# Performance work log

Measured on AMD Instinct MI355X. Metric: run time of the kernel, lower is better.

## Reference

```python
import jax, jax.numpy as jnp
import numpy as np

B, X, Z, E = 65536, 362, 100, 3  # batch, x_dim, z_dim, action_space


def _lin_init(k, fan_in, fan_out):
    kw, kb = jax.random.split(k)
    bound = 1.0 / np.sqrt(fan_in)
    W = jax.random.uniform(kw, (fan_in, fan_out), jnp.float32, -bound, bound)
    b = jax.random.uniform(kb, (fan_out,), jnp.float32, -bound, bound)
    return W, b


def setup_inputs() -> dict:
    key = jax.random.key(0)
    ks = jax.random.split(key, 12)
    batch_x = jax.random.normal(ks[0], (B, X), jnp.float32)
    batch_next = jax.random.normal(ks[1], (B, X), jnp.float32)
    batch_a = jax.random.randint(ks[2], (B,), 0, E, jnp.int32)
    # encoder params
    W1, b1 = _lin_init(ks[3], X, 256)
    W2, b2 = _lin_init(ks[4], 256, 200)
    W3, b3 = _lin_init(ks[5], 200, Z)
    # stacked expert params [E, in, out]
    def stack(k, fi, fo):
        kk = jax.random.split(k, E)
        Ws, bs = zip(*[_lin_init(kk[i], fi, fo) for i in range(E)])
        return jnp.stack(Ws), jnp.stack(bs)
    eW1, eb1 = stack(ks[6], Z, 150)
    eW2, eb2 = stack(ks[7], 150, 250)
    eW3, eb3 = stack(ks[8], 250, 300)
    eW4, eb4 = stack(ks[9], 300, X)
    return dict(batch_x=batch_x, batch_next=batch_next, batch_a=batch_a,
                W1=W1, b1=b1, W2=W2, b2=b2, W3=W3, b3=b3,
                eW1=eW1, eb1=eb1, eW2=eW2, eb2=eb2,
                eW3=eW3, eb3=eb3, eW4=eW4, eb4=eb4)


def reference(batch_x, batch_next, batch_a,
              W1, b1, W2, b2, W3, b3,
              eW1, eb1, eW2, eb2, eW3, eb3, eW4, eb4):
    # encoder: Linear->ReLU->Linear->ReLU->Linear->Sigmoid
    h = jax.nn.relu(batch_x @ W1 + b1)
    h = jax.nn.relu(h @ W2 + b2)
    z = jax.nn.sigmoid(h @ W3 + b3)  # [B, Z]
    # routed experts: run all E experts on the full batch (E=3, small),
    # then select per-sample output by action index (same math as per-sample loop)
    h = jax.nn.relu(jnp.einsum('bz,ezh->ebh', z, eW1) + eb1[:, None, :])
    h = jax.nn.relu(jnp.einsum('ebh,ehk->ebk', h, eW2) + eb2[:, None, :])
    h = jax.nn.relu(jnp.einsum('ebk,ekm->ebm', h, eW3) + eb3[:, None, :])
    pred_all = jnp.einsum('ebm,emx->ebx', h, eW4) + eb4[:, None, :]  # [E, B, X]
    pred = pred_all[batch_a, jnp.arange(batch_a.shape[0])]  # [B, X]
    delta = batch_next - batch_x
    loss = jnp.mean((pred[:, 1:] - delta[:, 1:]) ** 2) \
         + jnp.mean((pred[:, 0] - delta[:, 0]) ** 2)
    return loss
```

## Files before the change

### kernel.cpp

```cpp
#include <hip/hip_runtime.h>
#include <math.h>

#define BATCH 65536
#define XD 362
#define ZD 100

#define WS_IDX_OFF 256
#define WS_WT_OFF  786688

#define OFF_W1 0
#define OFF_W2 98304
#define OFF_W3 163840
#define OFF_E1 192512
#define OFF_E2 290816
#define OFF_E3 413696
#define OFF_E4 708608

#define ROWS 48

typedef short short8 __attribute__((ext_vector_type(8)));
typedef float f32x4 __attribute__((ext_vector_type(4)));

__device__ __forceinline__ unsigned short f2bf(float f) {
    union { float f; unsigned u; } v; v.f = f;
    unsigned u = v.u + 0x7fffu + ((v.u >> 16) & 1u);
    return (unsigned short)(u >> 16);
}
__device__ __forceinline__ float bf2f(unsigned u) {
    union { unsigned u; float f; } v; v.u = u << 16; return v.f;
}

__global__ __launch_bounds__(256) void repack_kernel(
    const float* __restrict__ W1, const float* __restrict__ W2,
    const float* __restrict__ W3, const float* __restrict__ eW1,
    const float* __restrict__ eW2, const float* __restrict__ eW3,
    const float* __restrict__ eW4, unsigned short* __restrict__ dst) {
    int m = blockIdx.y;
    const float* src; int K, N, Kp, Np; size_t off;
    if (m == 0)      { src = W1; K = 362; N = 256; Kp = 384; Np = 256; off = OFF_W1; }
    else if (m == 1) { src = W2; K = 256; N = 200; Kp = 256; Np = 256; off = OFF_W2; }
    else if (m == 2) { src = W3; K = 200; N = 100; Kp = 224; Np = 128; off = OFF_W3; }
    else if (m <= 5) { int e = m - 3;  src = eW1 + e * 15000;  K = 100; N = 150; Kp = 128; Np = 256; off = OFF_E1 + (size_t)e * 32768; }
    else if (m <= 8) { int e = m - 6;  src = eW2 + e * 37500;  K = 150; N = 250; Kp = 160; Np = 256; off = OFF_E2 + (size_t)e * 40960; }
    else if (m <= 11){ int e = m - 9;  src = eW3 + e * 75000;  K = 250; N = 300; Kp = 256; Np = 384; off = OFF_E3 + (size_t)e * 98304; }
    else             { int e = m - 12; src = eW4 + e * 108600; K = 300; N = 362; Kp = 320; Np = 384; off = OFF_E4 + (size_t)e * 122880; }
    int nkt = Kp / 32;
    int total = Kp * Np;
    for (int i = blockIdx.x * 256 + threadIdx.x; i < total; i += gridDim.x * 256) {
        int j = i & 7, lane = (i >> 3) & 63, t = i >> 9;
        int kt = t % nkt, ct = t / nkt;
        int k = kt * 32 + (lane >> 4) * 8 + j;
        int n = ct * 16 + (lane & 15);
        float v = (k < K && n < N) ? src[(size_t)k * N + n] : 0.0f;
        dst[off + i] = f2bf(v);
    }
}

__global__ __launch_bounds__(256) void bucket_kernel(const int* __restrict__ a,
                                                     int* __restrict__ counts,
                                                     int* __restrict__ idxlist) {
    int b = blockIdx.x * 256 + threadIdx.x;
    int lane = threadIdx.x & 63;
    int e = a[b];
    unsigned long long below = (lane == 63) ? ~0ull >> 1
                                            : ((1ull << (lane + 1)) - 1ull) >> 1;
    int pos = 0;
#pragma unroll
    for (int ee = 0; ee < 3; ++ee) {
        unsigned long long mask = __ballot(e == ee);
        if (e == ee) {
            int leader = __ffsll((long long)mask) - 1;
            int base = 0;
            if (lane == leader)
                base = atomicAdd(&counts[ee], __popcll(mask));
            base = __shfl(base, leader, 64);
            pos = base + __popcll(mask & below);
        }
    }
    idxlist[e * BATCH + pos] = b;
}

template <int KP, int NP, int LDI, int LDO, int NREAL, int NSTORE>
__device__ __forceinline__ void mfma_layer(
    const unsigned short* __restrict__ Wf, const float* __restrict__ bias,
    const unsigned short* __restrict__ inL, unsigned short* __restrict__ outL,
    int wv, int lane) {
    constexpr int NKT = KP / 32, NCT = NP / 16, CPW = NCT / 8;
    const int quad = lane >> 4, l15 = lane & 15;
    f32x4 acc[3][CPW];
#pragma unroll
    for (int rt = 0; rt < 3; ++rt)
#pragma unroll
        for (int i = 0; i < CPW; ++i) acc[rt][i] = (f32x4){0.f, 0.f, 0.f, 0.f};
    const unsigned short* ap = inL + l15 * LDI + quad * 8;
    __builtin_amdgcn_s_setprio(1);
#pragma unroll
    for (int kt = 0; kt < NKT; ++kt) {
        short8 a0 = *(const short8*)(ap + kt * 32);
        short8 a1 = *(const short8*)(ap + 16 * LDI + kt * 32);
        short8 a2 = *(const short8*)(ap + 32 * LDI + kt * 32);
        short8 bf[CPW];
#pragma unroll
        for (int i = 0; i < CPW; ++i)
            bf[i] = *(const short8*)(Wf + ((size_t)((wv + 8 * i) * NKT + kt) * 64 + lane) * 8);
#pragma unroll
        for (int i = 0; i < CPW; ++i) {
            acc[0][i] = __builtin_amdgcn_mfma_f32_16x16x32_bf16(a0, bf[i], acc[0][i], 0, 0, 0);
            acc[1][i] = __builtin_amdgcn_mfma_f32_16x16x32_bf16(a1, bf[i], acc[1][i], 0, 0, 0);
            acc[2][i] = __builtin_amdgcn_mfma_f32_16x16x32_bf16(a2, bf[i], acc[2][i], 0, 0, 0);
        }
    }
    __builtin_amdgcn_s_setprio(0);
#pragma unroll
    for (int i = 0; i < CPW; ++i) {
        int n = (wv + 8 * i) * 16 + l15;
        if (n < NSTORE) {
            float bv = (n < NREAL) ? bias[n] : 0.f;
#pragma unroll
            for (int rt = 0; rt < 3; ++rt)
#pragma unroll
                for (int r = 0; r < 4; ++r) {
                    int row = rt * 16 + quad * 4 + r;
                    float v = fmaxf(acc[rt][i][r] + bv, 0.f);
                    outL[row * LDO + n] = (n < NREAL) ? f2bf(v) : (unsigned short)0;
                }
        }
    }
}

__global__ __launch_bounds__(512, 4) void fused_kernel(
    const float* __restrict__ x, const float* __restrict__ xn,
    const int* __restrict__ counts, const int* __restrict__ idxlist,
    const unsigned short* __restrict__ Wts,
    const float* __restrict__ b1, const float* __restrict__ b2,
    const float* __restrict__ b3, const float* __restrict__ eb1,
    const float* __restrict__ eb2, const float* __restrict__ eb3,
    const float* __restrict__ eb4, float* __restrict__ out) {
    int e = blockIdx.y;
    int cnt = counts[e];
    int start = blockIdx.x * ROWS;
    if (start >= cnt) return;
    int nrows = min(ROWS, cnt - start);

    __shared__ unsigned short A[ROWS * 392];
    __shared__ unsigned short B[ROWS * 264];
    __shared__ int s_idx[ROWS];
    __shared__ float s_part[8];

    int tid = threadIdx.x;
    int wv = tid >> 6, lane = tid & 63;
    const int quad = lane >> 4, l15 = lane & 15;

    if (tid < ROWS)
        s_idx[tid] = (tid < nrows) ? idxlist[e * BATCH + start + tid] : -1;
    __syncthreads();

    {
        unsigned* dA = (unsigned*)A;
        for (int i = tid; i < ROWS * 196; i += 512) {
            int r = i / 196, c = i - r * 196;
            int b = s_idx[r];
            unsigned pk = 0u;
            if (c < 181 && b >= 0) {
                float2 v = *(const float2*)(x + (size_t)b * 362 + 2 * c);
                pk = (unsigned)f2bf(v.x) | ((unsigned)f2bf(v.y) << 16);
            }
            dA[i] = pk;
        }
    }
    __syncthreads();
    mfma_layer<384, 256, 392, 264, 256, 256>(Wts + OFF_W1, b1, A, B, wv, lane);
    __syncthreads();
    mfma_layer<256, 256, 264, 264, 200, 224>(Wts + OFF_W2, b2, B, A, wv, lane);
    __syncthreads();
    {
        const unsigned short* W3f = Wts + OFF_W3;
        f32x4 acc3[3];
#pragma unroll
        for (int rt = 0; rt < 3; ++rt) acc3[rt] = (f32x4){0.f, 0.f, 0.f, 0.f};
        const unsigned short* ap = A + l15 * 264 + quad * 8;
        __builtin_amdgcn_s_setprio(1);
#pragma unroll
        for (int kt = 0; kt < 7; ++kt) {
            short8 a0 = *(const short8*)(ap + kt * 32);
            short8 a1 = *(const short8*)(ap + 16 * 264 + kt * 32);
            short8 a2 = *(const short8*)(ap + 32 * 264 + kt * 32);
            short8 bf = *(const short8*)(W3f + ((size_t)(wv * 7 + kt) * 64 + lane) * 8);
            acc3[0] = __builtin_amdgcn_mfma_f32_16x16x32_bf16(a0, bf, acc3[0], 0, 0, 0);
            acc3[1] = __builtin_amdgcn_mfma_f32_16x16x32_bf16(a1, bf, acc3[1], 0, 0, 0);
            acc3[2] = __builtin_amdgcn_mfma_f32_16x16x32_bf16(a2, bf, acc3[2], 0, 0, 0);
        }
        __builtin_amdgcn_s_setprio(0);
        int n = wv * 16 + l15;
        float bv = (n < 100) ? b3[n] : 0.f;
#pragma unroll
        for (int rt = 0; rt < 3; ++rt)
#pragma unroll
            for (int r = 0; r < 4; ++r) {
                int row = rt * 16 + quad * 4 + r;
                float s = 1.0f / (1.0f + expf(-(acc3[rt][r] + bv)));
                B[row * 136 + n] = (n < 100) ? f2bf(s) : (unsigned short)0;
            }
    }
    __syncthreads();
    mfma_layer<128, 256, 136, 168, 150, 160>(Wts + OFF_E1 + (size_t)e * 32768,
                                             eb1 + e * 150, B, A, wv, lane);
    __syncthreads();
    mfma_layer<160, 256, 168, 264, 250, 256>(Wts + OFF_E2 + (size_t)e * 40960,
                                             eb2 + e * 250, A, B, wv, lane);
    __syncthreads();
    mfma_layer<256, 384, 264, 328, 300, 320>(Wts + OFF_E3 + (size_t)e * 98304,
                                             eb3 + e * 300, B, A, wv, lane);
    __syncthreads();

    float lacc = 0.0f;
    {
        constexpr int NKT = 10, CPW = 3;
        const unsigned short* Wf = Wts + OFF_E4 + (size_t)e * 122880;
        const float* bias4 = eb4 + (size_t)e * 362;
        f32x4 acc[3][CPW];
#pragma unroll
        for (int rt = 0; rt < 3; ++rt)
#pragma unroll
            for (int i = 0; i < CPW; ++i) acc[rt][i] = (f32x4){0.f, 0.f, 0.f, 0.f};
        const unsigned short* ap = A + l15 * 328 + quad * 8;
        __builtin_amdgcn_s_setprio(1);
#pragma unroll
        for (int kt = 0; kt < NKT; ++kt) {
            short8 a0 = *(const short8*)(ap + kt * 32);
            short8 a1 = *(const short8*)(ap + 16 * 328 + kt * 32);
            short8 a2 = *(const short8*)(ap + 32 * 328 + kt * 32);
            short8 bf[CPW];
#pragma unroll
            for (int i = 0; i < CPW; ++i)
                bf[i] = *(const short8*)(Wf + ((size_t)((wv + 8 * i) * NKT + kt) * 64 + lane) * 8);
#pragma unroll
            for (int i = 0; i < CPW; ++i) {
                acc[0][i] = __builtin_amdgcn_mfma_f32_16x16x32_bf16(a0, bf[i], acc[0][i], 0, 0, 0);
                acc[1][i] = __builtin_amdgcn_mfma_f32_16x16x32_bf16(a1, bf[i], acc[1][i], 0, 0, 0);
                acc[2][i] = __builtin_amdgcn_mfma_f32_16x16x32_bf16(a2, bf[i], acc[2][i], 0, 0, 0);
            }
        }
        __builtin_amdgcn_s_setprio(0);
        const float WC0 = 1.0f / 65536.0f;
        const float WCR = 1.0f / (361.0f * 65536.0f);
#pragma unroll
        for (int i = 0; i < CPW; ++i) {
            int n = (wv + 8 * i) * 16 + l15;
            if (n < 362) {
                float bv = bias4[n];
                float wgt = (n == 0) ? WC0 : WCR;
#pragma unroll
                for (int rt = 0; rt < 3; ++rt)
#pragma unroll
                    for (int r = 0; r < 4; ++r) {
                        int row = rt * 16 + quad * 4 + r;
                        int b = s_idx[row];
                        if (b >= 0) {
                            size_t o = (size_t)b * 362 + n;
                            float delta = xn[o] - x[o];
                            float err = acc[rt][i][r] + bv - delta;
                            lacc += wgt * err * err;
                        }
                    }
            }
        }
    }
    for (int off = 32; off; off >>= 1)
        lacc += __shfl_down(lacc, off, 64);
    if ((tid & 63) == 0) s_part[wv] = lacc;
    __syncthreads();
    if (tid == 0) {
        float s = 0.f;
#pragma unroll
        for (int i = 0; i < 8; ++i) s += s_part[i];
        atomicAdd(out, s);
    }
}

extern "C" void kernel_launch(void* const* d_in, const int* in_sizes, int n_in,
                              void* d_out, int out_size, void* d_ws, size_t ws_size,
                              hipStream_t stream) {
    const float* x   = (const float*)d_in[0];
    const float* xn  = (const float*)d_in[1];
    const int*   a   = (const int*)d_in[2];
    const float* W1  = (const float*)d_in[3];
    const float* b1  = (const float*)d_in[4];
    const float* W2  = (const float*)d_in[5];
    const float* b2  = (const float*)d_in[6];
    const float* W3  = (const float*)d_in[7];
    const float* b3  = (const float*)d_in[8];
    const float* eW1 = (const float*)d_in[9];
    const float* eb1 = (const float*)d_in[10];
    const float* eW2 = (const float*)d_in[11];
    const float* eb2 = (const float*)d_in[12];
    const float* eW3 = (const float*)d_in[13];
    const float* eb3 = (const float*)d_in[14];
    const float* eW4 = (const float*)d_in[15];
    const float* eb4 = (const float*)d_in[16];

    char* ws = (char*)d_ws;
    int* counts           = (int*)ws;
    int* idxlist          = (int*)(ws + WS_IDX_OFF);
    unsigned short* Wts   = (unsigned short*)(ws + WS_WT_OFF);

    hipMemsetAsync(counts, 0, 256, stream);
    hipMemsetAsync(d_out, 0, sizeof(float), stream);

    repack_kernel<<<dim3(32, 15), 256, 0, stream>>>(W1, W2, W3, eW1, eW2, eW3, eW4, Wts);
    bucket_kernel<<<BATCH / 256, 256, 0, stream>>>(a, counts, idxlist);
    fused_kernel<<<dim3((BATCH + ROWS - 1) / ROWS, 3), 512, 0, stream>>>(
        x, xn, counts, idxlist, Wts, b1, b2, b3, eb1, eb2, eb3, eb4, (float*)d_out);
}
```

Baseline: 420.1 us.

## Shrink row tile to 32, swap MFMA operands for packed stores, raise occupancy

Cuts the per-block row tile from 48 to 32, which shrinks shared memory and the accumulator registers. The launch-bounds occupancy hint rises from 4 to 6 blocks. The MFMA A/B operands are swapped so each lane holds 4 consecutive output columns of one row. That lets activations be written to LDS as packed 64-bit stores and the loss epilogue read x/xn with float2 loads. The trade-off is less weight reuse per block (weights are reloaded for every 32 rows instead of 48) and more blocks in flight.

```diff
diff --git a/kernel.cpp b/kernel.cpp
--- a/kernel.cpp
+++ b/kernel.cpp
@@ -16,10 +16,11 @@
 #define OFF_E3 413696
 #define OFF_E4 708608
 
-#define ROWS 48
+#define ROWS 32
 
 typedef short short8 __attribute__((ext_vector_type(8)));
 typedef float f32x4 __attribute__((ext_vector_type(4)));
+typedef unsigned u32x2 __attribute__((ext_vector_type(2)));
 
 __device__ __forceinline__ unsigned short f2bf(float f) {
     union { float f; unsigned u; } v; v.f = f;
@@ -87,9 +88,9 @@
     int wv, int lane) {
     constexpr int NKT = KP / 32, NCT = NP / 16, CPW = NCT / 8;
     const int quad = lane >> 4, l15 = lane & 15;
-    f32x4 acc[3][CPW];
-#pragma unroll
-    for (int rt = 0; rt < 3; ++rt)
+    f32x4 acc[2][CPW];
+#pragma unroll
+    for (int rt = 0; rt < 2; ++rt)
 #pragma unroll
         for (int i = 0; i < CPW; ++i) acc[rt][i] = (f32x4){0.f, 0.f, 0.f, 0.f};
     const unsigned short* ap = inL + l15 * LDI + quad * 8;
@@ -98,37 +99,44 @@
     for (int kt = 0; kt < NKT; ++kt) {
         short8 a0 = *(const short8*)(ap + kt * 32);
         short8 a1 = *(const short8*)(ap + 16 * LDI + kt * 32);
-        short8 a2 = *(const short8*)(ap + 32 * LDI + kt * 32);
         short8 bf[CPW];
 #pragma unroll
         for (int i = 0; i < CPW; ++i)
             bf[i] = *(const short8*)(Wf + ((size_t)((wv + 8 * i) * NKT + kt) * 64 + lane) * 8);
 #pragma unroll
         for (int i = 0; i < CPW; ++i) {
-            acc[0][i] = __builtin_amdgcn_mfma_f32_16x16x32_bf16(a0, bf[i], acc[0][i], 0, 0, 0);
-            acc[1][i] = __builtin_amdgcn_mfma_f32_16x16x32_bf16(a1, bf[i], acc[1][i], 0, 0, 0);
-            acc[2][i] = __builtin_amdgcn_mfma_f32_16x16x32_bf16(a2, bf[i], acc[2][i], 0, 0, 0);
+            acc[0][i] = __builtin_amdgcn_mfma_f32_16x16x32_bf16(bf[i], a0, acc[0][i], 0, 0, 0);
+            acc[1][i] = __builtin_amdgcn_mfma_f32_16x16x32_bf16(bf[i], a1, acc[1][i], 0, 0, 0);
         }
     }
     __builtin_amdgcn_s_setprio(0);
 #pragma unroll
     for (int i = 0; i < CPW; ++i) {
-        int n = (wv + 8 * i) * 16 + l15;
-        if (n < NSTORE) {
-            float bv = (n < NREAL) ? bias[n] : 0.f;
-#pragma unroll
-            for (int rt = 0; rt < 3; ++rt)
+        int nbase = (wv + 8 * i) * 16 + quad * 4;
+        if (nbase < NSTORE) {
+            float bv[4];
+#pragma unroll
+            for (int r = 0; r < 4; ++r)
+                bv[r] = (nbase + r < NREAL) ? bias[nbase + r] : 0.f;
+#pragma unroll
+            for (int rt = 0; rt < 2; ++rt) {
+                int row = rt * 16 + l15;
+                unsigned short h[4];
 #pragma unroll
                 for (int r = 0; r < 4; ++r) {
-                    int row = rt * 16 + quad * 4 + r;
-                    float v = fmaxf(acc[rt][i][r] + bv, 0.f);
-                    outL[row * LDO + n] = (n < NREAL) ? f2bf(v) : (unsigned short)0;
+                    float v = fmaxf(acc[rt][i][r] + bv[r], 0.f);
+                    h[r] = (nbase + r < NREAL) ? f2bf(v) : (unsigned short)0;
                 }
-        }
-    }
-}
-
-__global__ __launch_bounds__(512, 4) void fused_kernel(
+                u32x2 pk;
+                pk[0] = (unsigned)h[0] | ((unsigned)h[1] << 16);
+                pk[1] = (unsigned)h[2] | ((unsigned)h[3] << 16);
+                *(u32x2*)(outL + row * LDO + nbase) = pk;
+            }
+        }
+    }
+}
+
+__global__ __launch_bounds__(512, 6) void fused_kernel(
     const float* __restrict__ x, const float* __restrict__ xn,
     const int* __restrict__ counts, const int* __restrict__ idxlist,
     const unsigned short* __restrict__ Wts,
@@ -175,32 +183,39 @@
     __syncthreads();
     {
         const unsigned short* W3f = Wts + OFF_W3;
-        f32x4 acc3[3];
-#pragma unroll
-        for (int rt = 0; rt < 3; ++rt) acc3[rt] = (f32x4){0.f, 0.f, 0.f, 0.f};
+        f32x4 acc3[2];
+#pragma unroll
+        for (int rt = 0; rt < 2; ++rt) acc3[rt] = (f32x4){0.f, 0.f, 0.f, 0.f};
         const unsigned short* ap = A + l15 * 264 + quad * 8;
         __builtin_amdgcn_s_setprio(1);
 #pragma unroll
         for (int kt = 0; kt < 7; ++kt) {
             short8 a0 = *(const short8*)(ap + kt * 32);
             short8 a1 = *(const short8*)(ap + 16 * 264 + kt * 32);
-            short8 a2 = *(const short8*)(ap + 32 * 264 + kt * 32);
             short8 bf = *(const short8*)(W3f + ((size_t)(wv * 7 + kt) * 64 + lane) * 8);
-            acc3[0] = __builtin_amdgcn_mfma_f32_16x16x32_bf16(a0, bf, acc3[0], 0, 0, 0);
-            acc3[1] = __builtin_amdgcn_mfma_f32_16x16x32_bf16(a1, bf, acc3[1], 0, 0, 0);
-            acc3[2] = __builtin_amdgcn_mfma_f32_16x16x32_bf16(a2, bf, acc3[2], 0, 0, 0);
+            acc3[0] = __builtin_amdgcn_mfma_f32_16x16x32_bf16(bf, a0, acc3[0], 0, 0, 0);
+            acc3[1] = __builtin_amdgcn_mfma_f32_16x16x32_bf16(bf, a1, acc3[1], 0, 0, 0);
         }
         __builtin_amdgcn_s_setprio(0);
-        int n = wv * 16 + l15;
-        float bv = (n < 100) ? b3[n] : 0.f;
-#pragma unroll
-        for (int rt = 0; rt < 3; ++rt)
+        int nbase = wv * 16 + quad * 4;
+        float bv[4];
+#pragma unroll
+        for (int r = 0; r < 4; ++r)
+            bv[r] = (nbase + r < 100) ? b3[nbase + r] : 0.f;
+#pragma unroll
+        for (int rt = 0; rt < 2; ++rt) {
+            int row = rt * 16 + l15;
+            unsigned short h[4];
 #pragma unroll
             for (int r = 0; r < 4; ++r) {
-                int row = rt * 16 + quad * 4 + r;
-                float s = 1.0f / (1.0f + expf(-(acc3[rt][r] + bv)));
-                B[row * 136 + n] = (n < 100) ? f2bf(s) : (unsigned short)0;
-            }
+                float s = 1.0f / (1.0f + expf(-(acc3[rt][r] + bv[r])));
+                h[r] = (nbase + r < 100) ? f2bf(s) : (unsigned short)0;
+            }
+            u32x2 pk;
+            pk[0] = (unsigned)h[0] | ((unsigned)h[1] << 16);
+            pk[1] = (unsigned)h[2] | ((unsigned)h[3] << 16);
+            *(u32x2*)(B + row * 136 + nbase) = pk;
+        }
     }
     __syncthreads();
     mfma_layer<128, 256, 136, 168, 150, 160>(Wts + OFF_E1 + (size_t)e * 32768,
@@ -218,9 +233,9 @@
         constexpr int NKT = 10, CPW = 3;
         const unsigned short* Wf = Wts + OFF_E4 + (size_t)e * 122880;
         const float* bias4 = eb4 + (size_t)e * 362;
-        f32x4 acc[3][CPW];
-#pragma unroll
-        for (int rt = 0; rt < 3; ++rt)
+        f32x4 acc[2][CPW];
+#pragma unroll
+        for (int rt = 0; rt < 2; ++rt)
 #pragma unroll
             for (int i = 0; i < CPW; ++i) acc[rt][i] = (f32x4){0.f, 0.f, 0.f, 0.f};
         const unsigned short* ap = A + l15 * 328 + quad * 8;
@@ -229,16 +244,14 @@
         for (int kt = 0; kt < NKT; ++kt) {
             short8 a0 = *(const short8*)(ap + kt * 32);
             short8 a1 = *(const short8*)(ap + 16 * 328 + kt * 32);
-            short8 a2 = *(const short8*)(ap + 32 * 328 + kt * 32);
             short8 bf[CPW];
 #pragma unroll
             for (int i = 0; i < CPW; ++i)
                 bf[i] = *(const short8*)(Wf + ((size_t)((wv + 8 * i) * NKT + kt) * 64 + lane) * 8);
 #pragma unroll
             for (int i = 0; i < CPW; ++i) {
-                acc[0][i] = __builtin_amdgcn_mfma_f32_16x16x32_bf16(a0, bf[i], acc[0][i], 0, 0, 0);
-                acc[1][i] = __builtin_amdgcn_mfma_f32_16x16x32_bf16(a1, bf[i], acc[1][i], 0, 0, 0);
-                acc[2][i] = __builtin_amdgcn_mfma_f32_16x16x32_bf16(a2, bf[i], acc[2][i], 0, 0, 0);
+                acc[0][i] = __builtin_amdgcn_mfma_f32_16x16x32_bf16(bf[i], a0, acc[0][i], 0, 0, 0);
+                acc[1][i] = __builtin_amdgcn_mfma_f32_16x16x32_bf16(bf[i], a1, acc[1][i], 0, 0, 0);
             }
         }
         __builtin_amdgcn_s_setprio(0);
@@ -246,23 +259,33 @@
         const float WCR = 1.0f / (361.0f * 65536.0f);
 #pragma unroll
         for (int i = 0; i < CPW; ++i) {
-            int n = (wv + 8 * i) * 16 + l15;
-            if (n < 362) {
-                float bv = bias4[n];
-                float wgt = (n == 0) ? WC0 : WCR;
-#pragma unroll
-                for (int rt = 0; rt < 3; ++rt)
-#pragma unroll
-                    for (int r = 0; r < 4; ++r) {
-                        int row = rt * 16 + quad * 4 + r;
-                        int b = s_idx[row];
-                        if (b >= 0) {
-                            size_t o = (size_t)b * 362 + n;
-                            float delta = xn[o] - x[o];
-                            float err = acc[rt][i][r] + bv - delta;
-                            lacc += wgt * err * err;
+            int nbase = (wv + 8 * i) * 16 + quad * 4;
+            if (nbase < 362) {
+                bool p1 = nbase + 2 < 362;
+                float bv0 = bias4[nbase], bv1 = bias4[nbase + 1];
+                float bv2 = p1 ? bias4[nbase + 2] : 0.f;
+                float bv3 = p1 ? bias4[nbase + 3] : 0.f;
+                float w0 = (nbase == 0) ? WC0 : WCR;
+#pragma unroll
+                for (int rt = 0; rt < 2; ++rt) {
+                    int b = s_idx[rt * 16 + l15];
+                    if (b >= 0) {
+                        const float* xp  = x  + (size_t)b * 362 + nbase;
+                        const float* xnp = xn + (size_t)b * 362 + nbase;
+                        float2 xa  = *(const float2*)xp;
+                        float2 xna = *(const float2*)xnp;
+                        float e0 = acc[rt][i][0] + bv0 - (xna.x - xa.x);
+                        float e1 = acc[rt][i][1] + bv1 - (xna.y - xa.y);
+                        lacc += w0 * e0 * e0 + WCR * e1 * e1;
+                        if (p1) {
+                            float2 xb  = *(const float2*)(xp + 2);
+                            float2 xnb = *(const float2*)(xnp + 2);
+                            float e2 = acc[rt][i][2] + bv2 - (xnb.x - xb.x);
+                            float e3 = acc[rt][i][3] + bv3 - (xnb.y - xb.y);
+                            lacc += WCR * (e2 * e2 + e3 * e3);
                         }
                     }
+                }
             }
         }
     }
```

Result: faster. 400.4 us (-4.7%).
